# Kernel tuning notes

Hardware: AMD Instinct MI355X
Metric: run time of the kernel (lower is better)

Reference implementation:

```python
import jax, jax.numpy as jnp
import numpy as np

C_S, C_HID, H, P, V = 128, 16, 12, 4, 8
EPS = 1e-08
SOFTPLUS_INV_1 = 0.541324854612918


def _pts_from_linear(x, n_pts):
    # torch: split [..., 3*n] into 3 chunks of n, stack on dim=-1 -> [..., n, 3]
    B, N = x.shape[:2]
    return jnp.moveaxis(x.reshape(B, N, 3, n_pts), -2, -1)


def setup_inputs() -> dict:
    key = jax.random.key(0)
    ks = jax.random.split(key, 16)
    B, N = 2, 512
    hc = H * C_HID            # 192
    hpq = H * P * 3           # 144
    hpkv = H * (P + V) * 3    # 432
    cat_dim = H * (C_HID + V * 4)  # 576
    sc = 0.02
    inp = {
        "s": jax.random.normal(ks[0], (B, N, C_S), jnp.float32),
        "R": jax.random.normal(ks[1], (B, N, 3, 3), jnp.float32),
        "t": jax.random.normal(ks[2], (B, N, 3), jnp.float32),
        "pair_mask": jnp.ones((B, N, N), jnp.float32),
        "Wq": jax.random.normal(ks[3], (C_S, hc), jnp.float32) * sc,
        "bq": jnp.zeros((hc,), jnp.float32),
        "Wkv": jax.random.normal(ks[4], (C_S, 2 * hc), jnp.float32) * sc,
        "bkv": jnp.zeros((2 * hc,), jnp.float32),
        "Wqp": jax.random.normal(ks[5], (C_S, hpq), jnp.float32) * sc,
        "bqp": jnp.zeros((hpq,), jnp.float32),
        "Wkvp": jax.random.normal(ks[6], (C_S, hpkv), jnp.float32) * sc,
        "bkvp": jnp.zeros((hpkv,), jnp.float32),
        "head_weights": jnp.full((H,), SOFTPLUS_INV_1, jnp.float32),
        "Wout": jax.random.normal(ks[7], (cat_dim, C_S), jnp.float32) * sc,
        "bout": jnp.zeros((C_S,), jnp.float32),
    }
    return inp


def reference(s, R, t, pair_mask, Wq, bq, Wkv, bkv, Wqp, bqp, Wkvp, bkvp,
              head_weights, Wout, bout):
    B, N, _ = s.shape
    # scalar q/k/v
    q = (s @ Wq + bq).reshape(B, N, H, C_HID)
    kv = (s @ Wkv + bkv).reshape(B, N, H, 2 * C_HID)
    k, v = kv[..., :C_HID], kv[..., C_HID:]

    # point q/k/v in global frame: R x + t
    qp = _pts_from_linear(s @ Wqp + bqp, H * P)           # [B,N,HP,3]
    qp = jnp.einsum('bnij,bnpj->bnpi', R, qp) + t[:, :, None]
    qp = qp.reshape(B, N, H, P, 3)
    kvp = _pts_from_linear(s @ Wkvp + bkvp, H * (P + V))  # [B,N,H(P+V),3]
    kvp = jnp.einsum('bnij,bnpj->bnpi', R, kvp) + t[:, :, None]
    kvp = kvp.reshape(B, N, H, P + V, 3)
    kp, vp = kvp[..., :P, :], kvp[..., P:, :]

    # scalar attention logits [B,H,N,N]
    a = jnp.einsum('bihc,bjhc->bhij', q, k) * (1.0 / np.sqrt(3 * C_HID))

    # point-distance bias: sum_p ||q_i - k_j||^2 via |q|^2+|k|^2-2q.k
    sq_q = jnp.sum(qp * qp, axis=(-1, -2))   # [B,N,H]
    sq_k = jnp.sum(kp * kp, axis=(-1, -2))   # [B,N,H]
    cross = jnp.einsum('bihpc,bjhpc->bhij', qp, kp)
    d2 = (jnp.swapaxes(sq_q, 1, 2)[..., :, None]
          + jnp.swapaxes(sq_k, 1, 2)[..., None, :]
          - 2.0 * cross)                      # [B,H,N,N]
    hw = jax.nn.softplus(head_weights) * np.sqrt(1.0 / (3 * (P * 9.0 / 2)))
    pt_att = d2 * hw[None, :, None, None] * (-0.5)

    square_mask = 100000.0 * (pair_mask - 1.0)            # [B,N,N]
    a = jax.nn.softmax(a + pt_att + square_mask[:, None], axis=-1)

    # scalar output
    o = jnp.einsum('bhij,bjhc->bihc', a, v).reshape(B, N, H * C_HID)

    # point output, rotated back to local frame: R^T (x - t) form -> R^T x - t
    o_pt = jnp.einsum('bhij,bjhvc->bihvc', a, vp)         # [B,N,H,V,3]
    o_pt = jnp.einsum('bnji,bnhvj->bnhvi', R, o_pt) - t[:, :, None, None]
    o_pt_norm = jnp.sqrt(jnp.sum(o_pt * o_pt, axis=-1) + EPS).reshape(B, N, H * V)
    o_pt_flat = o_pt.reshape(B, N, H * V, 3)

    cat = jnp.concatenate(
        [o, o_pt_flat[..., 0], o_pt_flat[..., 1], o_pt_flat[..., 2], o_pt_norm],
        axis=-1)                                           # [B,N,576]
    return cat @ Wout + bout
```

## Files before the change

### kernel.cpp

```cpp
#include <hip/hip_runtime.h>
#include <hip/hip_bf16.h>
#include <math.h>

#define H_    12
#define B_    2
#define N_    512
#define BH_   (B_*H_)
#define QSCALE 0.14433756729740643f
#define CPT_K  0.13608276348795434f

#define OFF_WPP  1245184
#define OFF_WOP  1318912
#define OFF_BIA  1355776
#define OFF_QB   1356928
#define OFF_KP   1553536
#define OFF_VP   1750144
#define OFF_SA   2045056
#define OFF_SB   2057344
#define OFF_CATP 2069632

typedef __attribute__((ext_vector_type(8))) short sh8;
typedef __attribute__((ext_vector_type(4))) float f32x4;
typedef unsigned short u16t;

static __device__ __forceinline__ u16t f2b(float x) {
    __hip_bfloat16 h = __float2bfloat16(x);
    return *reinterpret_cast<u16t*>(&h);
}
static __device__ __forceinline__ int catp_idx(int tok, int col) {
    return (tok >> 4)*9216 + (col >> 5)*512 + ((col >> 3) & 3)*128
         + (tok & 15)*8 + (col & 7);
}

__global__ __launch_bounds__(256) void convert_kernel(
    const float* __restrict__ Wq,  const float* __restrict__ bq,
    const float* __restrict__ Wkv, const float* __restrict__ bkv,
    const float* __restrict__ Wqp, const float* __restrict__ bqp,
    const float* __restrict__ Wkvp,const float* __restrict__ bkvp,
    const float* __restrict__ Wout, float* __restrict__ ws)
{
    const int g = blockIdx.x * 256 + threadIdx.x;
    union { sh8 v; u16t u[8]; } pk;

    if (g < 18432) {
        int u = g;
        int n = u & 63, kq = (u >> 6) & 3, ks = (u >> 8) & 3, nt = u >> 10;
        int col = nt*64 + n, k0 = ks*32 + kq*8;
        const float* w; int lc, od;
        if (col < 192)      { w = Wq;   lc = col;     od = 192; }
        else if (col < 576) { w = Wkv;  lc = col-192; od = 384; }
        else if (col < 720) { w = Wqp;  lc = col-576; od = 144; }
        else                { w = Wkvp; lc = col-720; od = 432; }
        #pragma unroll
        for (int j = 0; j < 8; ++j) pk.u[j] = f2b(w[(k0+j)*od + lc]);
        *((sh8*)((u16t*)(ws + OFF_WPP)) + u) = pk.v;
    } else if (g < 27648) {
        int u = g - 18432;
        int n = u & 63, kq = (u >> 6) & 3, rem = u >> 8;
        int ks = rem % 18, nt = rem / 18;
        int col = nt*64 + n, k0 = ks*32 + kq*8;
        #pragma unroll
        for (int j = 0; j < 8; ++j) pk.u[j] = f2b(Wout[(k0+j)*128 + col]);
        *((sh8*)((u16t*)(ws + OFF_WOP)) + u) = pk.v;
    } else if (g < 28800) {
        int col = g - 27648;
        float bv;
        if (col < 192)      bv = bq[col];
        else if (col < 576) bv = bkv[col-192];
        else if (col < 720) bv = bqp[col-576];
        else                bv = bkvp[col-720];
        ws[OFF_BIA + col] = bv;
    }
}

__global__ __launch_bounds__(512) void projpack_kernel(
    const float* __restrict__ s,
    const float* __restrict__ Rg, const float* __restrict__ tg,
    const float* __restrict__ hwg, float* __restrict__ ws)
{
    __shared__ float ldsP[8][1160];

    u16t* Qb = (u16t*)(ws + OFF_QB);
    u16t* Kp = (u16t*)(ws + OFF_KP);
    u16t* Vp = (u16t*)(ws + OFF_VP);
    float* sa_g = ws + OFF_SA;
    float* sb_g = ws + OFF_SB;

    const int tid  = threadIdx.x;
    const int w    = tid >> 6, lane = tid & 63;
    const int kq   = lane >> 4, lx = lane & 15;
    const int tok0 = blockIdx.x * 8;
    const int b    = tok0 >> 9, n0 = tok0 & 511;

    sh8 afr[4];
    #pragma unroll
    for (int ks = 0; ks < 4; ++ks) {
        const float* src = s + (tok0 + (lx & 7))*128 + ks*32 + kq*8;
        float4 u0 = *(const float4*)(src);
        float4 u1 = *(const float4*)(src+4);
        union { sh8 v; u16t u[8]; } pk;
        pk.u[0]=f2b(u0.x); pk.u[1]=f2b(u0.y); pk.u[2]=f2b(u0.z); pk.u[3]=f2b(u0.w);
        pk.u[4]=f2b(u1.x); pk.u[5]=f2b(u1.y); pk.u[6]=f2b(u1.z); pk.u[7]=f2b(u1.w);
        afr[ks] = pk.v;
    }

    const sh8* Bp = (const sh8*)((const u16t*)(ws + OFF_WPP));
    const float* bias = ws + OFF_BIA;

    #pragma unroll 3
    for (int g = 0; g < 9; ++g) {
        int gg = w*9 + g;
        int nt = gg >> 2, nq = gg & 3;
        f32x4 acc = {0.f,0.f,0.f,0.f};
        #pragma unroll
        for (int ks = 0; ks < 4; ++ks) {
            sh8 bf = Bp[((nt*4 + ks)*4 + kq)*64 + nq*16 + lx];
            acc = __builtin_amdgcn_mfma_f32_16x16x32_bf16(afr[ks], bf, acc, 0, 0, 0);
        }
        float bv = bias[gg*16 + lx];
        if (kq < 2) {
            #pragma unroll
            for (int r = 0; r < 4; ++r)
                ldsP[kq*4 + r][gg*16 + lx] = acc[r] + bv;
        }
    }
    __syncthreads();

    for (int idx = tid; idx < 8*48; idx += 512) {
        int tk = idx / 48, p = idx % 48;
        int tok = tok0 + tk;
        const float* Rr = Rg + tok*9;
        const float* tr = tg + tok*3;
        float x0 = ldsP[tk][576 +  0 + p];
        float x1 = ldsP[tk][576 + 48 + p];
        float x2 = ldsP[tk][576 + 96 + p];
        ldsP[tk][576 +  0 + p] = Rr[0]*x0 + Rr[1]*x1 + Rr[2]*x2 + tr[0];
        ldsP[tk][576 + 48 + p] = Rr[3]*x0 + Rr[4]*x1 + Rr[5]*x2 + tr[1];
        ldsP[tk][576 + 96 + p] = Rr[6]*x0 + Rr[7]*x1 + Rr[8]*x2 + tr[2];
    }
    for (int idx = tid; idx < 8*144; idx += 512) {
        int tk = idx / 144, p = idx % 144;
        int tok = tok0 + tk;
        const float* Rr = Rg + tok*9;
        const float* tr = tg + tok*3;
        float x0 = ldsP[tk][720 +   0 + p];
        float x1 = ldsP[tk][720 + 144 + p];
        float x2 = ldsP[tk][720 + 288 + p];
        ldsP[tk][720 +   0 + p] = Rr[0]*x0 + Rr[1]*x1 + Rr[2]*x2 + tr[0];
        ldsP[tk][720 + 144 + p] = Rr[3]*x0 + Rr[4]*x1 + Rr[5]*x2 + tr[1];
        ldsP[tk][720 + 288 + p] = Rr[6]*x0 + Rr[7]*x1 + Rr[8]*x2 + tr[2];
    }
    __syncthreads();

    for (int idx = tid; idx < 8*24; idx += 512) {
        int tk = idx / 24, r2 = idx % 24, h = r2 >> 1, half = r2 & 1;
        float hx = hwg[h];
        float sp = (hx > 20.f) ? hx : log1pf(__expf(hx));
        float c_pt = -0.5f * sp * CPT_K;
        union { sh8 v[2]; u16t u[16]; } pk;
        if (half == 0) {
            #pragma unroll
            for (int e = 0; e < 16; ++e) pk.u[e] = f2b(ldsP[tk][h*16 + e] * QSCALE);
        } else {
            float qs = -2.f * c_pt;
            #pragma unroll
            for (int e = 0; e < 12; ++e)
                pk.u[e] = f2b(ldsP[tk][576 + (e%3)*48 + h*4 + e/3] * qs);
            pk.u[12]=0; pk.u[13]=0; pk.u[14]=0; pk.u[15]=0;
        }
        u16t* dst = Qb + ((b*H_+h)*N_ + n0 + tk)*32 + half*16;
        *(sh8*)dst = pk.v[0];
        *(sh8*)(dst+8) = pk.v[1];
    }
    for (int idx = tid; idx < 8*48; idx += 512) {
        int tk = idx / 48, r2 = idx % 48, h = r2 >> 2, fq = r2 & 3;
        int j = n0 + tk, bh = b*H_ + h;
        union { sh8 v; u16t u[8]; } pk;
        #pragma unroll
        for (int e = 0; e < 8; ++e) {
            int c = fq*8 + e;
            float val;
            if (c < 16)      val = ldsP[tk][192 + h*32 + c];
            else if (c < 28) val = ldsP[tk][720 + ((c-16)%3)*144 + h*12 + (c-16)/3];
            else             val = 0.f;
            pk.u[e] = f2b(val);
        }
        *(sh8*)(Kp + bh*16384 + (j>>4)*512 + fq*128 + (j&15)*8) = pk.v;
    }
    for (int idx = tid; idx < 480; idx += 512) {
        int h = idx / 40, d = idx % 40;
        int bh = b*H_ + h;
        union { sh8 v; u16t u[8]; } pk;
        #pragma unroll
        for (int e = 0; e < 8; ++e) {
            float val;
            if (d < 16) val = ldsP[e][192 + h*32 + 16 + d];
            else        val = ldsP[e][720 + ((d-16)%3)*144 + h*12 + 4 + (d-16)/3];
            pk.u[e] = f2b(val);
        }
        int j = n0;
        *(sh8*)(Vp + bh*24576 + (j>>5)*1536 + (d>>4)*512 + ((j>>3)&3)*128
                + (d&15)*8) = pk.v;
    }
    for (int idx = tid; idx < 8*12; idx += 512) {
        int tk = idx / 12, h = idx % 12;
        float hx = hwg[h];
        float sp = (hx > 20.f) ? hx : log1pf(__expf(hx));
        float c_pt = -0.5f * sp * CPT_K;
        float sq = 0.f, sk = 0.f;
        #pragma unroll
        for (int pp = 0; pp < 4; ++pp)
            #pragma unroll
            for (int c = 0; c < 3; ++c) {
                float a = ldsP[tk][576 + c*48  + h*4  + pp]; sq += a*a;
                float k = ldsP[tk][720 + c*144 + h*12 + pp]; sk += k*k;
            }
        sa_g[(b*H_+h)*N_ + n0 + tk] = c_pt * sq;
        sb_g[(b*H_+h)*N_ + n0 + tk] = c_pt * sk;
    }
}

__global__ __launch_bounds__(512, 2) void attn_kernel(
    const float* __restrict__ Rg, const float* __restrict__ tg,
    const float* __restrict__ maskg, float* __restrict__ ws)
{
    __shared__ u16t smP[8*16*72];
    __shared__ float mbuf[3*128*20];
    __shared__ float obuf[32*32];

    const u16t* Qb = (const u16t*)(ws + OFF_QB);
    const u16t* Kp = (const u16t*)(ws + OFF_KP);
    const u16t* Vp = (const u16t*)(ws + OFF_VP);
    const float* sa_g = ws + OFF_SA;
    const float* sb_g = ws + OFF_SB;
    u16t* catp = (u16t*)(ws + OFF_CATP);

    const int tid  = threadIdx.x;
    const int w    = tid >> 6, lane = tid & 63;
    const int rg   = w & 1, jh = w >> 1;
    const int kq   = lane >> 4, lx = lane & 15;
    const int bh   = blockIdx.x >> 4;
    const int it   = blockIdx.x & 15;
    const int b    = bh / H_, h = bh % H_;
    const int i0   = it * 32;

    sh8 qfrag = *(const sh8*)(Qb + (bh*N_ + i0 + rg*16 + lx)*32 + kq*8);
    float sa_r[4];
    #pragma unroll
    for (int r = 0; r < 4; ++r)
        sa_r[r] = sa_g[bh*N_ + i0 + rg*16 + kq*4 + r];

    float m_run[4] = {-1e30f,-1e30f,-1e30f,-1e30f};
    float l_run[4] = {0.f,0.f,0.f,0.f};
    f32x4 oc0 = {0.f,0.f,0.f,0.f}, oc1 = oc0, oc2 = oc0;

    const float* mrow = maskg + (size_t)(b*N_ + i0 + rg*16 + kq*4)*N_ + lx;
    u16t* pw = smP + w*1152;

    #pragma unroll
    for (int t = 0; t < 2; ++t) {
        const int jt = jh*2 + t;
        const int j0 = jt * 64;

        f32x4 sc[4];
        #pragma unroll
        for (int st = 0; st < 4; ++st) {
            sh8 kf = *(const sh8*)(Kp + bh*16384 + (jt*4+st)*512 + kq*128 + lx*8);
            f32x4 z = {0.f,0.f,0.f,0.f};
            sc[st] = __builtin_amdgcn_mfma_f32_16x16x32_bf16(qfrag, kf, z, 0, 0, 0);
        }
        float sbv[4];
        #pragma unroll
        for (int st = 0; st < 4; ++st) sbv[st] = sb_g[bh*N_ + j0 + st*16 + lx];
        float mb[16];
        #pragma unroll
        for (int r = 0; r < 4; ++r)
            #pragma unroll
            for (int st = 0; st < 4; ++st)
                mb[r*4+st] = mrow[r*N_ + j0 + st*16];

        float L[16];
        #pragma unroll
        for (int st = 0; st < 4; ++st)
            #pragma unroll
            for (int r = 0; r < 4; ++r)
                L[st*4+r] = sc[st][r] + sa_r[r] + sbv[st] + 1e5f*(mb[r*4+st] - 1.f);

        #pragma unroll
        for (int r = 0; r < 4; ++r) {
            float tm = fmaxf(fmaxf(L[0*4+r], L[1*4+r]), fmaxf(L[2*4+r], L[3*4+r]));
            tm = fmaxf(tm, __shfl_xor(tm, 1));
            tm = fmaxf(tm, __shfl_xor(tm, 2));
            tm = fmaxf(tm, __shfl_xor(tm, 4));
            tm = fmaxf(tm, __shfl_xor(tm, 8));
            float mnew = fmaxf(m_run[r], tm);
            float al = __expf(m_run[r] - mnew);
            m_run[r] = mnew;
            l_run[r] *= al;
            oc0[r] *= al; oc1[r] *= al; oc2[r] *= al;
        }
        #pragma unroll
        for (int st = 0; st < 4; ++st)
            #pragma unroll
            for (int r = 0; r < 4; ++r) {
                float p = __expf(L[st*4+r] - m_run[r]);
                l_run[r] += p;
                pw[(kq*4+r)*72 + st*16 + lx] = f2b(p);
            }
        #pragma unroll
        for (int c = 0; c < 2; ++c) {
            sh8 pa = *(const sh8*)(pw + lx*72 + c*32 + kq*8);
            #pragma unroll
            for (int nq = 0; nq < 3; ++nq) {
                sh8 vf = *(const sh8*)(Vp + bh*24576 + (jt*2+c)*1536 + nq*512
                                        + kq*128 + lx*8);
                if (nq == 0) oc0 = __builtin_amdgcn_mfma_f32_16x16x32_bf16(pa, vf, oc0, 0,0,0);
                if (nq == 1) oc1 = __builtin_amdgcn_mfma_f32_16x16x32_bf16(pa, vf, oc1, 0,0,0);
                if (nq == 2) oc2 = __builtin_amdgcn_mfma_f32_16x16x32_bf16(pa, vf, oc2, 0,0,0);
            }
        }
    }

    if (jh > 0) {
        float* mb = mbuf + ((jh-1)*128 + rg*64 + lane)*20;
        #pragma unroll
        for (int r = 0; r < 4; ++r) {
            mb[r]      = m_run[r];
            mb[4 + r]  = l_run[r];
            mb[8 + r]  = oc0[r];
            mb[12 + r] = oc1[r];
            mb[16 + r] = oc2[r];
        }
    }
    __syncthreads();
    if (jh == 0) {
        float linv[4];
        #pragma unroll
        for (int r = 0; r < 4; ++r) {
            float ms = m_run[r];
            #pragma unroll
            for (int q = 0; q < 3; ++q)
                ms = fmaxf(ms, mbuf[(q*128 + rg*64 + lane)*20 + r]);
            float eA = __expf(m_run[r] - ms);
            float l = l_run[r]*eA;
            oc0[r] *= eA; oc1[r] *= eA; oc2[r] *= eA;
            #pragma unroll
            for (int q = 0; q < 3; ++q) {
                const float* mb = mbuf + (q*128 + rg*64 + lane)*20;
                float e = __expf(mb[r] - ms);
                l      += mb[4+r]*e;
                oc0[r] += mb[8+r]*e;
                oc1[r] += mb[12+r]*e;
                oc2[r] += mb[16+r]*e;
            }
            l += __shfl_xor(l, 1); l += __shfl_xor(l, 2);
            l += __shfl_xor(l, 4); l += __shfl_xor(l, 8);
            linv[r] = 1.f / l;
        }

        #pragma unroll
        for (int r = 0; r < 4; ++r) {
            int tok = b*N_ + i0 + rg*16 + kq*4 + r;
            catp[catp_idx(tok, h*16 + lx)] = f2b(oc0[r] * linv[r]);
            obuf[(rg*16 + kq*4 + r)*32 + lx]      = oc1[r] * linv[r];
            obuf[(rg*16 + kq*4 + r)*32 + 16 + lx] = oc2[r] * linv[r];
        }

        #pragma unroll
        for (int tsk = 0; tsk < 2; ++tsk) {
            int task = lane + tsk*64;
            int r = task >> 3, pv = task & 7;
            int tok = b*N_ + i0 + rg*16 + r;
            const float* Rr = Rg + tok*9;
            const float* tr = tg + tok*3;
            float g0 = obuf[(rg*16 + r)*32 + pv*3 + 0];
            float g1 = obuf[(rg*16 + r)*32 + pv*3 + 1];
            float g2 = obuf[(rg*16 + r)*32 + pv*3 + 2];
            float px = Rr[0]*g0 + Rr[3]*g1 + Rr[6]*g2 - tr[0];
            float py = Rr[1]*g0 + Rr[4]*g1 + Rr[7]*g2 - tr[1];
            float pz = Rr[2]*g0 + Rr[5]*g1 + Rr[8]*g2 - tr[2];
            float nrm = sqrtf(px*px + py*py + pz*pz + 1e-8f);
            catp[catp_idx(tok, 192 + h*8 + pv)] = f2b(px);
            catp[catp_idx(tok, 288 + h*8 + pv)] = f2b(py);
            catp[catp_idx(tok, 384 + h*8 + pv)] = f2b(pz);
            catp[catp_idx(tok, 480 + h*8 + pv)] = f2b(nrm);
        }
    }
}

__global__ __launch_bounds__(512) void out_kernel(
    const float* __restrict__ bout, const float* __restrict__ ws,
    float* __restrict__ out)
{
    __shared__ float part[2][3][64][4];

    const int tid = threadIdx.x;
    const int w = tid >> 6, lane = tid & 63;
    const int cg = w & 1, kh = w >> 1;
    const int lx = lane & 15, kq = lane >> 4;
    const int nt = blockIdx.x, mt = blockIdx.y;

    const sh8* Ap = (const sh8*)((const u16t*)(ws + OFF_CATP));
    const sh8* Bp = (const sh8*)((const u16t*)(ws + OFF_WOP));

    const int ke0 = (kh*18) >> 2;
    const int ke1 = ((kh+1)*18) >> 2;

    f32x4 acc = {0.f,0.f,0.f,0.f};
    #pragma unroll 5
    for (int ks = ke0; ks < ke1; ++ks) {
        sh8 af = Ap[((mt*18 + ks)*4 + kq)*16 + lx];
        sh8 bf = Bp[(((nt>>1)*18 + ks)*4 + kq)*64 + (nt&1)*32 + cg*16 + lx];
        acc = __builtin_amdgcn_mfma_f32_16x16x32_bf16(af, bf, acc, 0, 0, 0);
    }
    if (kh > 0) {
        #pragma unroll
        for (int r = 0; r < 4; ++r) part[cg][kh-1][lane][r] = acc[r];
    }
    __syncthreads();
    if (kh == 0) {
        int col = nt*32 + cg*16 + lx;
        float bv = bout[col];
        #pragma unroll
        for (int r = 0; r < 4; ++r) {
            int row = mt*16 + kq*4 + r;
            out[row*128 + col] = acc[r] + part[cg][0][lane][r]
                               + part[cg][1][lane][r] + part[cg][2][lane][r] + bv;
        }
    }
}

extern "C" void kernel_launch(void* const* d_in, const int* in_sizes, int n_in,
                              void* d_out, int out_size, void* d_ws, size_t ws_size,
                              hipStream_t stream) {
    const float* s    = (const float*)d_in[0];
    const float* R    = (const float*)d_in[1];
    const float* t    = (const float*)d_in[2];
    const float* mask = (const float*)d_in[3];
    const float* Wq   = (const float*)d_in[4];
    const float* bq   = (const float*)d_in[5];
    const float* Wkv  = (const float*)d_in[6];
    const float* bkv  = (const float*)d_in[7];
    const float* Wqp  = (const float*)d_in[8];
    const float* bqp  = (const float*)d_in[9];
    const float* Wkvp = (const float*)d_in[10];
    const float* bkvp = (const float*)d_in[11];
    const float* hw   = (const float*)d_in[12];
    const float* Wout = (const float*)d_in[13];
    const float* bout = (const float*)d_in[14];
    float* ws  = (float*)d_ws;
    float* out = (float*)d_out;

    convert_kernel<<<113, 256, 0, stream>>>(Wq, bq, Wkv, bkv,
                                            Wqp, bqp, Wkvp, bkvp, Wout, ws);
    projpack_kernel<<<128, 512, 0, stream>>>(s, R, t, hw, ws);
    attn_kernel<<<BH_*16, 512, 0, stream>>>(R, t, mask, ws);
    out_kernel<<<dim3(4, 64), 512, 0, stream>>>(bout, ws, out);
}
```

Measured before the change: 109.8 us.

## Fuse four kernels into one persistent kernel with atomic grid barriers

Replaces the four separate launches (weight convert, projection/pack, attention, output GEMM) with a single persistent kernel of 384 blocks that separates the phases with a software grid barrier built on an atomic counter. The Wout conversion moves off the critical path and now runs alongside the projection phase. The aim is to remove the launch overhead and inter-kernel gaps of a small workload. The risk is deadlock if not all 384 blocks are co-resident, plus spin-wait cost and lower occupancy from the shared 53 KB LDS buffer and launch bounds.

```diff
diff --git a/kernel.cpp b/kernel.cpp
--- a/kernel.cpp
+++ b/kernel.cpp
@@ -6,6 +6,7 @@
 #define B_    2
 #define N_    512
 #define BH_   (B_*H_)
+#define NB_   384
 #define QSCALE 0.14433756729740643f
 #define CPT_K  0.13608276348795434f
 
@@ -23,6 +24,8 @@
 typedef __attribute__((ext_vector_type(4))) float f32x4;
 typedef unsigned short u16t;
 
+__device__ unsigned int g_bar = 0;
+
 static __device__ __forceinline__ u16t f2b(float x) {
     __hip_bfloat16 h = __float2bfloat16(x);
     return *reinterpret_cast<u16t*>(&h);
@@ -32,400 +35,415 @@
          + (tok & 15)*8 + (col & 7);
 }
 
-__global__ __launch_bounds__(256) void convert_kernel(
+static __device__ __forceinline__ void grid_barrier() {
+    __syncthreads();
+    if (threadIdx.x == 0) {
+        __threadfence();
+        unsigned t = atomicAdd(&g_bar, 1u);
+        unsigned target = t - (t % (unsigned)NB_) + (unsigned)NB_;
+        while (__hip_atomic_load(&g_bar, __ATOMIC_RELAXED,
+                                 __HIP_MEMORY_SCOPE_AGENT) < target)
+            __builtin_amdgcn_s_sleep(2);
+        __threadfence();
+    }
+    __syncthreads();
+}
+
+__global__ __launch_bounds__(512, 4) void fused_kernel(
+    const float* __restrict__ s,
+    const float* __restrict__ Rg, const float* __restrict__ tg,
+    const float* __restrict__ maskg,
     const float* __restrict__ Wq,  const float* __restrict__ bq,
     const float* __restrict__ Wkv, const float* __restrict__ bkv,
     const float* __restrict__ Wqp, const float* __restrict__ bqp,
     const float* __restrict__ Wkvp,const float* __restrict__ bkvp,
-    const float* __restrict__ Wout, float* __restrict__ ws)
+    const float* __restrict__ hwg,
+    const float* __restrict__ Wout, const float* __restrict__ bout,
+    float* __restrict__ ws, float* __restrict__ out)
 {
-    const int g = blockIdx.x * 256 + threadIdx.x;
-    union { sh8 v; u16t u[8]; } pk;
-
-    if (g < 18432) {
-        int u = g;
-        int n = u & 63, kq = (u >> 6) & 3, ks = (u >> 8) & 3, nt = u >> 10;
-        int col = nt*64 + n, k0 = ks*32 + kq*8;
-        const float* w; int lc, od;
-        if (col < 192)      { w = Wq;   lc = col;     od = 192; }
-        else if (col < 576) { w = Wkv;  lc = col-192; od = 384; }
-        else if (col < 720) { w = Wqp;  lc = col-576; od = 144; }
-        else                { w = Wkvp; lc = col-720; od = 432; }
-        #pragma unroll
-        for (int j = 0; j < 8; ++j) pk.u[j] = f2b(w[(k0+j)*od + lc]);
-        *((sh8*)((u16t*)(ws + OFF_WPP)) + u) = pk.v;
-    } else if (g < 27648) {
-        int u = g - 18432;
-        int n = u & 63, kq = (u >> 6) & 3, rem = u >> 8;
-        int ks = rem % 18, nt = rem / 18;
-        int col = nt*64 + n, k0 = ks*32 + kq*8;
-        #pragma unroll
-        for (int j = 0; j < 8; ++j) pk.u[j] = f2b(Wout[(k0+j)*128 + col]);
-        *((sh8*)((u16t*)(ws + OFF_WOP)) + u) = pk.v;
-    } else if (g < 28800) {
-        int col = g - 27648;
-        float bv;
-        if (col < 192)      bv = bq[col];
-        else if (col < 576) bv = bkv[col-192];
-        else if (col < 720) bv = bqp[col-576];
-        else                bv = bkvp[col-720];
-        ws[OFF_BIA + col] = bv;
-    }
-}
-
-__global__ __launch_bounds__(512) void projpack_kernel(
-    const float* __restrict__ s,
-    const float* __restrict__ Rg, const float* __restrict__ tg,
-    const float* __restrict__ hwg, float* __restrict__ ws)
-{
-    __shared__ float ldsP[8][1160];
-
-    u16t* Qb = (u16t*)(ws + OFF_QB);
-    u16t* Kp = (u16t*)(ws + OFF_KP);
-    u16t* Vp = (u16t*)(ws + OFF_VP);
-    float* sa_g = ws + OFF_SA;
-    float* sb_g = ws + OFF_SB;
+    __shared__ __align__(16) char ldsraw[53248];
 
     const int tid  = threadIdx.x;
+    const int bid  = blockIdx.x;
     const int w    = tid >> 6, lane = tid & 63;
     const int kq   = lane >> 4, lx = lane & 15;
-    const int tok0 = blockIdx.x * 8;
-    const int b    = tok0 >> 9, n0 = tok0 & 511;
-
-    sh8 afr[4];
-    #pragma unroll
-    for (int ks = 0; ks < 4; ++ks) {
-        const float* src = s + (tok0 + (lx & 7))*128 + ks*32 + kq*8;
-        float4 u0 = *(const float4*)(src);
-        float4 u1 = *(const float4*)(src+4);
-        union { sh8 v; u16t u[8]; } pk;
-        pk.u[0]=f2b(u0.x); pk.u[1]=f2b(u0.y); pk.u[2]=f2b(u0.z); pk.u[3]=f2b(u0.w);
-        pk.u[4]=f2b(u1.x); pk.u[5]=f2b(u1.y); pk.u[6]=f2b(u1.z); pk.u[7]=f2b(u1.w);
-        afr[ks] = pk.v;
+
+    if (w == 0 && bid < 306) {
+        int task = bid*64 + lane;
+        if (task < 18432) {
+            int u = task;
+            int n = u & 63, kq0 = (u >> 6) & 3, ks = (u >> 8) & 3, nt = u >> 10;
+            int col = nt*64 + n, k0 = ks*32 + kq0*8;
+            const float* wp; int lc, od;
+            if (col < 192)      { wp = Wq;   lc = col;     od = 192; }
+            else if (col < 576) { wp = Wkv;  lc = col-192; od = 384; }
+            else if (col < 720) { wp = Wqp;  lc = col-576; od = 144; }
+            else                { wp = Wkvp; lc = col-720; od = 432; }
+            union { sh8 v; u16t uu[8]; } pk;
+            #pragma unroll
+            for (int j = 0; j < 8; ++j) pk.uu[j] = f2b(wp[(k0+j)*od + lc]);
+            *((sh8*)((u16t*)(ws + OFF_WPP)) + u) = pk.v;
+        } else {
+            int col = task - 18432;
+            float bv;
+            if (col < 192)      bv = bq[col];
+            else if (col < 576) bv = bkv[col-192];
+            else if (col < 720) bv = bqp[col-576];
+            else                bv = bkvp[col-720];
+            ws[OFF_BIA + col] = bv;
+        }
     }
-
-    const sh8* Bp = (const sh8*)((const u16t*)(ws + OFF_WPP));
-    const float* bias = ws + OFF_BIA;
-
-    #pragma unroll 3
-    for (int g = 0; g < 9; ++g) {
-        int gg = w*9 + g;
-        int nt = gg >> 2, nq = gg & 3;
-        f32x4 acc = {0.f,0.f,0.f,0.f};
+    grid_barrier();
+
+    if (bid < 128) {
+        float (*ldsP)[1160] = reinterpret_cast<float(*)[1160]>(ldsraw);
+
+        u16t* Qb = (u16t*)(ws + OFF_QB);
+        u16t* Kp = (u16t*)(ws + OFF_KP);
+        u16t* Vp = (u16t*)(ws + OFF_VP);
+        float* sa_g = ws + OFF_SA;
+        float* sb_g = ws + OFF_SB;
+
+        const int tok0 = bid * 8;
+        const int b    = tok0 >> 9, n0 = tok0 & 511;
+
+        sh8 afr[4];
         #pragma unroll
         for (int ks = 0; ks < 4; ++ks) {
-            sh8 bf = Bp[((nt*4 + ks)*4 + kq)*64 + nq*16 + lx];
-            acc = __builtin_amdgcn_mfma_f32_16x16x32_bf16(afr[ks], bf, acc, 0, 0, 0);
-        }
-        float bv = bias[gg*16 + lx];
-        if (kq < 2) {
-            #pragma unroll
-            for (int r = 0; r < 4; ++r)
-                ldsP[kq*4 + r][gg*16 + lx] = acc[r] + bv;
-        }
+            const float* src = s + (tok0 + (lx & 7))*128 + ks*32 + kq*8;
+            float4 u0 = *(const float4*)(src);
+            float4 u1 = *(const float4*)(src+4);
+            union { sh8 v; u16t u[8]; } pk;
+            pk.u[0]=f2b(u0.x); pk.u[1]=f2b(u0.y); pk.u[2]=f2b(u0.z); pk.u[3]=f2b(u0.w);
+            pk.u[4]=f2b(u1.x); pk.u[5]=f2b(u1.y); pk.u[6]=f2b(u1.z); pk.u[7]=f2b(u1.w);
+            afr[ks] = pk.v;
+        }
+
+        const sh8* Bp = (const sh8*)((const u16t*)(ws + OFF_WPP));
+        const float* bias = ws + OFF_BIA;
+
+        #pragma unroll 3
+        for (int g = 0; g < 9; ++g) {
+            int gg = w*9 + g;
+            int nt = gg >> 2, nq = gg & 3;
+            f32x4 acc = {0.f,0.f,0.f,0.f};
+            #pragma unroll
+            for (int ks = 0; ks < 4; ++ks) {
+                sh8 bf = Bp[((nt*4 + ks)*4 + kq)*64 + nq*16 + lx];
+                acc = __builtin_amdgcn_mfma_f32_16x16x32_bf16(afr[ks], bf, acc, 0, 0, 0);
+            }
+            float bv = bias[gg*16 + lx];
+            if (kq < 2) {
+                #pragma unroll
+                for (int r = 0; r < 4; ++r)
+                    ldsP[kq*4 + r][gg*16 + lx] = acc[r] + bv;
+            }
+        }
+        __syncthreads();
+
+        for (int idx = tid; idx < 8*48; idx += 512) {
+            int tk = idx / 48, p = idx % 48;
+            int tok = tok0 + tk;
+            const float* Rr = Rg + tok*9;
+            const float* tr = tg + tok*3;
+            float x0 = ldsP[tk][576 +  0 + p];
+            float x1 = ldsP[tk][576 + 48 + p];
+            float x2 = ldsP[tk][576 + 96 + p];
+            ldsP[tk][576 +  0 + p] = Rr[0]*x0 + Rr[1]*x1 + Rr[2]*x2 + tr[0];
+            ldsP[tk][576 + 48 + p] = Rr[3]*x0 + Rr[4]*x1 + Rr[5]*x2 + tr[1];
+            ldsP[tk][576 + 96 + p] = Rr[6]*x0 + Rr[7]*x1 + Rr[8]*x2 + tr[2];
+        }
+        for (int idx = tid; idx < 8*144; idx += 512) {
+            int tk = idx / 144, p = idx % 144;
+            int tok = tok0 + tk;
+            const float* Rr = Rg + tok*9;
+            const float* tr = tg + tok*3;
+            float x0 = ldsP[tk][720 +   0 + p];
+            float x1 = ldsP[tk][720 + 144 + p];
+            float x2 = ldsP[tk][720 + 288 + p];
+            ldsP[tk][720 +   0 + p] = Rr[0]*x0 + Rr[1]*x1 + Rr[2]*x2 + tr[0];
+            ldsP[tk][720 + 144 + p] = Rr[3]*x0 + Rr[4]*x1 + Rr[5]*x2 + tr[1];
+            ldsP[tk][720 + 288 + p] = Rr[6]*x0 + Rr[7]*x1 + Rr[8]*x2 + tr[2];
+        }
+        __syncthreads();
+
+        for (int idx = tid; idx < 8*24; idx += 512) {
+            int tk = idx / 24, r2 = idx % 24, h = r2 >> 1, half = r2 & 1;
+            float hx = hwg[h];
+            float sp = (hx > 20.f) ? hx : log1pf(__expf(hx));
+            float c_pt = -0.5f * sp * CPT_K;
+            union { sh8 v[2]; u16t u[16]; } pk;
+            if (half == 0) {
+                #pragma unroll
+                for (int e = 0; e < 16; ++e) pk.u[e] = f2b(ldsP[tk][h*16 + e] * QSCALE);
+            } else {
+                float qs = -2.f * c_pt;
+                #pragma unroll
+                for (int e = 0; e < 12; ++e)
+                    pk.u[e] = f2b(ldsP[tk][576 + (e%3)*48 + h*4 + e/3] * qs);
+                pk.u[12]=0; pk.u[13]=0; pk.u[14]=0; pk.u[15]=0;
+            }
+            u16t* dst = Qb + ((b*H_+h)*N_ + n0 + tk)*32 + half*16;
+            *(sh8*)dst = pk.v[0];
+            *(sh8*)(dst+8) = pk.v[1];
+        }
+        for (int idx = tid; idx < 8*48; idx += 512) {
+            int tk = idx / 48, r2 = idx % 48, h = r2 >> 2, fq = r2 & 3;
+            int j = n0 + tk, bh = b*H_ + h;
+            union { sh8 v; u16t u[8]; } pk;
+            #pragma unroll
+            for (int e = 0; e < 8; ++e) {
+                int c = fq*8 + e;
+                float val;
+                if (c < 16)      val = ldsP[tk][192 + h*32 + c];
+                else if (c < 28) val = ldsP[tk][720 + ((c-16)%3)*144 + h*12 + (c-16)/3];
+                else             val = 0.f;
+                pk.u[e] = f2b(val);
+            }
+            *(sh8*)(Kp + bh*16384 + (j>>4)*512 + fq*128 + (j&15)*8) = pk.v;
+        }
+        for (int idx = tid; idx < 480; idx += 512) {
+            int h = idx / 40, d = idx % 40;
+            int bh = b*H_ + h;
+            union { sh8 v; u16t u[8]; } pk;
+            #pragma unroll
+            for (int e = 0; e < 8; ++e) {
+                float val;
+                if (d < 16) val = ldsP[e][192 + h*32 + 16 + d];
+                else        val = ldsP[e][720 + ((d-16)%3)*144 + h*12 + 4 + (d-16)/3];
+                pk.u[e] = f2b(val);
+            }
+            int j = n0;
+            *(sh8*)(Vp + bh*24576 + (j>>5)*1536 + (d>>4)*512 + ((j>>3)&3)*128
+                    + (d&15)*8) = pk.v;
+        }
+        for (int idx = tid; idx < 8*12; idx += 512) {
+            int tk = idx / 12, h = idx % 12;
+            float hx = hwg[h];
+            float sp = (hx > 20.f) ? hx : log1pf(__expf(hx));
+            float c_pt = -0.5f * sp * CPT_K;
+            float sq = 0.f, sk = 0.f;
+            #pragma unroll
+            for (int pp = 0; pp < 4; ++pp)
+                #pragma unroll
+                for (int c = 0; c < 3; ++c) {
+                    float a = ldsP[tk][576 + c*48  + h*4  + pp]; sq += a*a;
+                    float k = ldsP[tk][720 + c*144 + h*12 + pp]; sk += k*k;
+                }
+            sa_g[(b*H_+h)*N_ + n0 + tk] = c_pt * sq;
+            sb_g[(b*H_+h)*N_ + n0 + tk] = c_pt * sk;
+        }
+    } else if (bid < 272 && w == 0) {
+        int u = (bid - 128)*64 + lane;
+        int n = u & 63, kq0 = (u >> 6) & 3, rem = u >> 8;
+        int ks = rem % 18, nt = rem / 18;
+        int col = nt*64 + n, k0 = ks*32 + kq0*8;
+        union { sh8 v; u16t uu[8]; } pk;
+        #pragma unroll
+        for (int j = 0; j < 8; ++j) pk.uu[j] = f2b(Wout[(k0+j)*128 + col]);
+        *((sh8*)((u16t*)(ws + OFF_WOP)) + u) = pk.v;
     }
-    __syncthreads();
-
-    for (int idx = tid; idx < 8*48; idx += 512) {
-        int tk = idx / 48, p = idx % 48;
-        int tok = tok0 + tk;
-        const float* Rr = Rg + tok*9;
-        const float* tr = tg + tok*3;
-        float x0 = ldsP[tk][576 +  0 + p];
-        float x1 = ldsP[tk][576 + 48 + p];
-        float x2 = ldsP[tk][576 + 96 + p];
-        ldsP[tk][576 +  0 + p] = Rr[0]*x0 + Rr[1]*x1 + Rr[2]*x2 + tr[0];
-        ldsP[tk][576 + 48 + p] = Rr[3]*x0 + Rr[4]*x1 + Rr[5]*x2 + tr[1];
-        ldsP[tk][576 + 96 + p] = Rr[6]*x0 + Rr[7]*x1 + Rr[8]*x2 + tr[2];
-    }
-    for (int idx = tid; idx < 8*144; idx += 512) {
-        int tk = idx / 144, p = idx % 144;
-        int tok = tok0 + tk;
-        const float* Rr = Rg + tok*9;
-        const float* tr = tg + tok*3;
-        float x0 = ldsP[tk][720 +   0 + p];
-        float x1 = ldsP[tk][720 + 144 + p];
-        float x2 = ldsP[tk][720 + 288 + p];
-        ldsP[tk][720 +   0 + p] = Rr[0]*x0 + Rr[1]*x1 + Rr[2]*x2 + tr[0];
-        ldsP[tk][720 + 144 + p] = Rr[3]*x0 + Rr[4]*x1 + Rr[5]*x2 + tr[1];
-        ldsP[tk][720 + 288 + p] = Rr[6]*x0 + Rr[7]*x1 + Rr[8]*x2 + tr[2];
-    }
-    __syncthreads();
-
-    for (int idx = tid; idx < 8*24; idx += 512) {
-        int tk = idx / 24, r2 = idx % 24, h = r2 >> 1, half = r2 & 1;
-        float hx = hwg[h];
-        float sp = (hx > 20.f) ? hx : log1pf(__expf(hx));
-        float c_pt = -0.5f * sp * CPT_K;
-        union { sh8 v[2]; u16t u[16]; } pk;
-        if (half == 0) {
-            #pragma unroll
-            for (int e = 0; e < 16; ++e) pk.u[e] = f2b(ldsP[tk][h*16 + e] * QSCALE);
-        } else {
-            float qs = -2.f * c_pt;
-            #pragma unroll
-            for (int e = 0; e < 12; ++e)
-                pk.u[e] = f2b(ldsP[tk][576 + (e%3)*48 + h*4 + e/3] * qs);
-            pk.u[12]=0; pk.u[13]=0; pk.u[14]=0; pk.u[15]=0;
-        }
-        u16t* dst = Qb + ((b*H_+h)*N_ + n0 + tk)*32 + half*16;
-        *(sh8*)dst = pk.v[0];
-        *(sh8*)(dst+8) = pk.v[1];
-    }
-    for (int idx = tid; idx < 8*48; idx += 512) {
-        int tk = idx / 48, r2 = idx % 48, h = r2 >> 2, fq = r2 & 3;
-        int j = n0 + tk, bh = b*H_ + h;
-        union { sh8 v; u16t u[8]; } pk;
-        #pragma unroll
-        for (int e = 0; e < 8; ++e) {
-            int c = fq*8 + e;
-            float val;
-            if (c < 16)      val = ldsP[tk][192 + h*32 + c];
-            else if (c < 28) val = ldsP[tk][720 + ((c-16)%3)*144 + h*12 + (c-16)/3];
-            else             val = 0.f;
-            pk.u[e] = f2b(val);
-        }
-        *(sh8*)(Kp + bh*16384 + (j>>4)*512 + fq*128 + (j&15)*8) = pk.v;
-    }
-    for (int idx = tid; idx < 480; idx += 512) {
-        int h = idx / 40, d = idx % 40;
-        int bh = b*H_ + h;
-        union { sh8 v; u16t u[8]; } pk;
-        #pragma unroll
-        for (int e = 0; e < 8; ++e) {
-            float val;
-            if (d < 16) val = ldsP[e][192 + h*32 + 16 + d];
-            else        val = ldsP[e][720 + ((d-16)%3)*144 + h*12 + 4 + (d-16)/3];
-            pk.u[e] = f2b(val);
-        }
-        int j = n0;
-        *(sh8*)(Vp + bh*24576 + (j>>5)*1536 + (d>>4)*512 + ((j>>3)&3)*128
-                + (d&15)*8) = pk.v;
-    }
-    for (int idx = tid; idx < 8*12; idx += 512) {
-        int tk = idx / 12, h = idx % 12;
-        float hx = hwg[h];
-        float sp = (hx > 20.f) ? hx : log1pf(__expf(hx));
-        float c_pt = -0.5f * sp * CPT_K;
-        float sq = 0.f, sk = 0.f;
-        #pragma unroll
-        for (int pp = 0; pp < 4; ++pp)
-            #pragma unroll
-            for (int c = 0; c < 3; ++c) {
-                float a = ldsP[tk][576 + c*48  + h*4  + pp]; sq += a*a;
-                float k = ldsP[tk][720 + c*144 + h*12 + pp]; sk += k*k;
-            }
-        sa_g[(b*H_+h)*N_ + n0 + tk] = c_pt * sq;
-        sb_g[(b*H_+h)*N_ + n0 + tk] = c_pt * sk;
-    }
-}
-
-__global__ __launch_bounds__(512, 2) void attn_kernel(
-    const float* __restrict__ Rg, const float* __restrict__ tg,
-    const float* __restrict__ maskg, float* __restrict__ ws)
-{
-    __shared__ u16t smP[8*16*72];
-    __shared__ float mbuf[3*128*20];
-    __shared__ float obuf[32*32];
-
-    const u16t* Qb = (const u16t*)(ws + OFF_QB);
-    const u16t* Kp = (const u16t*)(ws + OFF_KP);
-    const u16t* Vp = (const u16t*)(ws + OFF_VP);
-    const float* sa_g = ws + OFF_SA;
-    const float* sb_g = ws + OFF_SB;
-    u16t* catp = (u16t*)(ws + OFF_CATP);
-
-    const int tid  = threadIdx.x;
-    const int w    = tid >> 6, lane = tid & 63;
-    const int rg   = w & 1, jh = w >> 1;
-    const int kq   = lane >> 4, lx = lane & 15;
-    const int bh   = blockIdx.x >> 4;
-    const int it   = blockIdx.x & 15;
-    const int b    = bh / H_, h = bh % H_;
-    const int i0   = it * 32;
-
-    sh8 qfrag = *(const sh8*)(Qb + (bh*N_ + i0 + rg*16 + lx)*32 + kq*8);
-    float sa_r[4];
-    #pragma unroll
-    for (int r = 0; r < 4; ++r)
-        sa_r[r] = sa_g[bh*N_ + i0 + rg*16 + kq*4 + r];
-
-    float m_run[4] = {-1e30f,-1e30f,-1e30f,-1e30f};
-    float l_run[4] = {0.f,0.f,0.f,0.f};
-    f32x4 oc0 = {0.f,0.f,0.f,0.f}, oc1 = oc0, oc2 = oc0;
-
-    const float* mrow = maskg + (size_t)(b*N_ + i0 + rg*16 + kq*4)*N_ + lx;
-    u16t* pw = smP + w*1152;
-
-    #pragma unroll
-    for (int t = 0; t < 2; ++t) {
-        const int jt = jh*2 + t;
-        const int j0 = jt * 64;
-
-        f32x4 sc[4];
-        #pragma unroll
-        for (int st = 0; st < 4; ++st) {
-            sh8 kf = *(const sh8*)(Kp + bh*16384 + (jt*4+st)*512 + kq*128 + lx*8);
-            f32x4 z = {0.f,0.f,0.f,0.f};
-            sc[st] = __builtin_amdgcn_mfma_f32_16x16x32_bf16(qfrag, kf, z, 0, 0, 0);
-        }
-        float sbv[4];
-        #pragma unroll
-        for (int st = 0; st < 4; ++st) sbv[st] = sb_g[bh*N_ + j0 + st*16 + lx];
-        float mb[16];
+    grid_barrier();
+
+    {
+        u16t* smP  = (u16t*)ldsraw;
+        float* mbuf = (float*)(ldsraw + 18432);
+        float* obuf = (float*)(ldsraw + 49152);
+
+        const u16t* Qb = (const u16t*)(ws + OFF_QB);
+        const u16t* Kp = (const u16t*)(ws + OFF_KP);
+        const u16t* Vp = (const u16t*)(ws + OFF_VP);
+        const float* sa_g = ws + OFF_SA;
+        const float* sb_g = ws + OFF_SB;
+        u16t* catp = (u16t*)(ws + OFF_CATP);
+
+        const int rg   = w & 1, jh = w >> 1;
+        const int bh   = bid >> 4;
+        const int it   = bid & 15;
+        const int b    = bh / H_, h = bh % H_;
+        const int i0   = it * 32;
+
+        sh8 qfrag = *(const sh8*)(Qb + (bh*N_ + i0 + rg*16 + lx)*32 + kq*8);
+        float sa_r[4];
         #pragma unroll
         for (int r = 0; r < 4; ++r)
+            sa_r[r] = sa_g[bh*N_ + i0 + rg*16 + kq*4 + r];
+
+        float m_run[4] = {-1e30f,-1e30f,-1e30f,-1e30f};
+        float l_run[4] = {0.f,0.f,0.f,0.f};
+        f32x4 oc0 = {0.f,0.f,0.f,0.f}, oc1 = oc0, oc2 = oc0;
+
+        const float* mrow = maskg + (size_t)(b*N_ + i0 + rg*16 + kq*4)*N_ + lx;
+        u16t* pw = smP + w*1152;
+
+        #pragma unroll
+        for (int t = 0; t < 2; ++t) {
+            const int jt = jh*2 + t;
+            const int j0 = jt * 64;
+
+            f32x4 sc[4];
+            #pragma unroll
+            for (int st = 0; st < 4; ++st) {
+                sh8 kf = *(const sh8*)(Kp + bh*16384 + (jt*4+st)*512 + kq*128 + lx*8);
+                f32x4 z = {0.f,0.f,0.f,0.f};
+                sc[st] = __builtin_amdgcn_mfma_f32_16x16x32_bf16(qfrag, kf, z, 0, 0, 0);
+            }
+            float sbv[4];
+            #pragma unroll
+            for (int st = 0; st < 4; ++st) sbv[st] = sb_g[bh*N_ + j0 + st*16 + lx];
+            float mb[16];
+            #pragma unroll
+            for (int r = 0; r < 4; ++r)
+                #pragma unroll
+                for (int st = 0; st < 4; ++st)
+                    mb[r*4+st] = mrow[r*N_ + j0 + st*16];
+
+            float L[16];
             #pragma unroll
             for (int st = 0; st < 4; ++st)
-                mb[r*4+st] = mrow[r*N_ + j0 + st*16];
-
-        float L[16];
-        #pragma unroll
-        for (int st = 0; st < 4; ++st)
+                #pragma unroll
+                for (int r = 0; r < 4; ++r)
+                    L[st*4+r] = sc[st][r] + sa_r[r] + sbv[st] + 1e5f*(mb[r*4+st] - 1.f);
+
+            #pragma unroll
+            for (int r = 0; r < 4; ++r) {
+                float tm = fmaxf(fmaxf(L[0*4+r], L[1*4+r]), fmaxf(L[2*4+r], L[3*4+r]));
+                tm = fmaxf(tm, __shfl_xor(tm, 1));
+                tm = fmaxf(tm, __shfl_xor(tm, 2));
+                tm = fmaxf(tm, __shfl_xor(tm, 4));
+                tm = fmaxf(tm, __shfl_xor(tm, 8));
+                float mnew = fmaxf(m_run[r], tm);
+                float al = __expf(m_run[r] - mnew);
+                m_run[r] = mnew;
+                l_run[r] *= al;
+                oc0[r] *= al; oc1[r] *= al; oc2[r] *= al;
+            }
+            #pragma unroll
+            for (int st = 0; st < 4; ++st)
+                #pragma unroll
+                for (int r = 0; r < 4; ++r) {
+                    float p = __expf(L[st*4+r] - m_run[r]);
+                    l_run[r] += p;
+                    pw[(kq*4+r)*72 + st*16 + lx] = f2b(p);
+                }
+            #pragma unroll
+            for (int c = 0; c < 2; ++c) {
+                sh8 pa = *(const sh8*)(pw + lx*72 + c*32 + kq*8);
+                #pragma unroll
+                for (int nq = 0; nq < 3; ++nq) {
+                    sh8 vf = *(const sh8*)(Vp + bh*24576 + (jt*2+c)*1536 + nq*512
+                                            + kq*128 + lx*8);
+                    if (nq == 0) oc0 = __builtin_amdgcn_mfma_f32_16x16x32_bf16(pa, vf, oc0, 0,0,0);
+                    if (nq == 1) oc1 = __builtin_amdgcn_mfma_f32_16x16x32_bf16(pa, vf, oc1, 0,0,0);
+                    if (nq == 2) oc2 = __builtin_amdgcn_mfma_f32_16x16x32_bf16(pa, vf, oc2, 0,0,0);
+                }
+            }
+        }
+
+        if (jh > 0) {
+            float* mb = mbuf + ((jh-1)*128 + rg*64 + lane)*20;
+            #pragma unroll
+            for (int r = 0; r < 4; ++r) {
+                mb[r]      = m_run[r];
+                mb[4 + r]  = l_run[r];
+                mb[8 + r]  = oc0[r];
+                mb[12 + r] = oc1[r];
+                mb[16 + r] = oc2[r];
+            }
+        }
+        __syncthreads();
+        if (jh == 0) {
+            float linv[4];
+            #pragma unroll
+            for (int r = 0; r < 4; ++r) {
+                float ms = m_run[r];
+                #pragma unroll
+                for (int q = 0; q < 3; ++q)
+                    ms = fmaxf(ms, mbuf[(q*128 + rg*64 + lane)*20 + r]);
+                float eA = __expf(m_run[r] - ms);
+                float l = l_run[r]*eA;
+                oc0[r] *= eA; oc1[r] *= eA; oc2[r] *= eA;
+                #pragma unroll
+                for (int q = 0; q < 3; ++q) {
+                    const float* mb = mbuf + (q*128 + rg*64 + lane)*20;
+                    float e = __expf(mb[r] - ms);
+                    l      += mb[4+r]*e;
+                    oc0[r] += mb[8+r]*e;
+                    oc1[r] += mb[12+r]*e;
+                    oc2[r] += mb[16+r]*e;
+                }
+                l += __shfl_xor(l, 1); l += __shfl_xor(l, 2);
+                l += __shfl_xor(l, 4); l += __shfl_xor(l, 8);
+                linv[r] = 1.f / l;
+            }
+
+            #pragma unroll
+            for (int r = 0; r < 4; ++r) {
+                int tok = b*N_ + i0 + rg*16 + kq*4 + r;
+                catp[catp_idx(tok, h*16 + lx)] = f2b(oc0[r] * linv[r]);
+                obuf[(rg*16 + kq*4 + r)*32 + lx]      = oc1[r] * linv[r];
+                obuf[(rg*16 + kq*4 + r)*32 + 16 + lx] = oc2[r] * linv[r];
+            }
+
+            #pragma unroll
+            for (int tsk = 0; tsk < 2; ++tsk) {
+                int task = lane + tsk*64;
+                int r = task >> 3, pv = task & 7;
+                int tok = b*N_ + i0 + rg*16 + r;
+                const float* Rr = Rg + tok*9;
+                const float* tr = tg + tok*3;
+                float g0 = obuf[(rg*16 + r)*32 + pv*3 + 0];
+                float g1 = obuf[(rg*16 + r)*32 + pv*3 + 1];
+                float g2 = obuf[(rg*16 + r)*32 + pv*3 + 2];
+                float px = Rr[0]*g0 + Rr[3]*g1 + Rr[6]*g2 - tr[0];
+                float py = Rr[1]*g0 + Rr[4]*g1 + Rr[7]*g2 - tr[1];
+                float pz = Rr[2]*g0 + Rr[5]*g1 + Rr[8]*g2 - tr[2];
+                float nrm = sqrtf(px*px + py*py + pz*pz + 1e-8f);
+                catp[catp_idx(tok, 192 + h*8 + pv)] = f2b(px);
+                catp[catp_idx(tok, 288 + h*8 + pv)] = f2b(py);
+                catp[catp_idx(tok, 384 + h*8 + pv)] = f2b(pz);
+                catp[catp_idx(tok, 480 + h*8 + pv)] = f2b(nrm);
+            }
+        }
+    }
+    grid_barrier();
+
+    if (bid < 256) {
+        float* part = (float*)ldsraw;
+
+        const int cg = w & 1, kh = w >> 1;
+        const int nt = bid & 3, mt = bid >> 2;
+
+        const sh8* Ap = (const sh8*)((const u16t*)(ws + OFF_CATP));
+        const sh8* Bp = (const sh8*)((const u16t*)(ws + OFF_WOP));
+
+        const int ke0 = (kh*18) >> 2;
+        const int ke1 = ((kh+1)*18) >> 2;
+
+        f32x4 acc = {0.f,0.f,0.f,0.f};
+        #pragma unroll 5
+        for (int ks = ke0; ks < ke1; ++ks) {
+            sh8 af = Ap[((mt*18 + ks)*4 + kq)*16 + lx];
+            sh8 bf = Bp[(((nt>>1)*18 + ks)*4 + kq)*64 + (nt&1)*32 + cg*16 + lx];
+            acc = __builtin_amdgcn_mfma_f32_16x16x32_bf16(af, bf, acc, 0, 0, 0);
+        }
+        if (kh > 0) {
             #pragma unroll
             for (int r = 0; r < 4; ++r)
-                L[st*4+r] = sc[st][r] + sa_r[r] + sbv[st] + 1e5f*(mb[r*4+st] - 1.f);
-
-        #pragma unroll
-        for (int r = 0; r < 4; ++r) {
-            float tm = fmaxf(fmaxf(L[0*4+r], L[1*4+r]), fmaxf(L[2*4+r], L[3*4+r]));
-            tm = fmaxf(tm, __shfl_xor(tm, 1));
-            tm = fmaxf(tm, __shfl_xor(tm, 2));
-            tm = fmaxf(tm, __shfl_xor(tm, 4));
-            tm = fmaxf(tm, __shfl_xor(tm, 8));
-            float mnew = fmaxf(m_run[r], tm);
-            float al = __expf(m_run[r] - mnew);
-            m_run[r] = mnew;
-            l_run[r] *= al;
-            oc0[r] *= al; oc1[r] *= al; oc2[r] *= al;
-        }
-        #pragma unroll
-        for (int st = 0; st < 4; ++st)
+                part[((cg*3 + (kh-1))*64 + lane)*4 + r] = acc[r];
+        }
+        __syncthreads();
+        if (kh == 0) {
+            int col = nt*32 + cg*16 + lx;
+            float bv = bout[col];
             #pragma unroll
             for (int r = 0; r < 4; ++r) {
-                float p = __expf(L[st*4+r] - m_run[r]);
-                l_run[r] += p;
-                pw[(kq*4+r)*72 + st*16 + lx] = f2b(p);
-            }
-        #pragma unroll
-        for (int c = 0; c < 2; ++c) {
-            sh8 pa = *(const sh8*)(pw + lx*72 + c*32 + kq*8);
-            #pragma unroll
-            for (int nq = 0; nq < 3; ++nq) {
-                sh8 vf = *(const sh8*)(Vp + bh*24576 + (jt*2+c)*1536 + nq*512
-                                        + kq*128 + lx*8);
-                if (nq == 0) oc0 = __builtin_amdgcn_mfma_f32_16x16x32_bf16(pa, vf, oc0, 0,0,0);
-                if (nq == 1) oc1 = __builtin_amdgcn_mfma_f32_16x16x32_bf16(pa, vf, oc1, 0,0,0);
-                if (nq == 2) oc2 = __builtin_amdgcn_mfma_f32_16x16x32_bf16(pa, vf, oc2, 0,0,0);
-            }
-        }
-    }
-
-    if (jh > 0) {
-        float* mb = mbuf + ((jh-1)*128 + rg*64 + lane)*20;
-        #pragma unroll
-        for (int r = 0; r < 4; ++r) {
-            mb[r]      = m_run[r];
-            mb[4 + r]  = l_run[r];
-            mb[8 + r]  = oc0[r];
-            mb[12 + r] = oc1[r];
-            mb[16 + r] = oc2[r];
-        }
-    }
-    __syncthreads();
-    if (jh == 0) {
-        float linv[4];
-        #pragma unroll
-        for (int r = 0; r < 4; ++r) {
-            float ms = m_run[r];
-            #pragma unroll
-            for (int q = 0; q < 3; ++q)
-                ms = fmaxf(ms, mbuf[(q*128 + rg*64 + lane)*20 + r]);
-            float eA = __expf(m_run[r] - ms);
-            float l = l_run[r]*eA;
-            oc0[r] *= eA; oc1[r] *= eA; oc2[r] *= eA;
-            #pragma unroll
-            for (int q = 0; q < 3; ++q) {
-                const float* mb = mbuf + (q*128 + rg*64 + lane)*20;
-                float e = __expf(mb[r] - ms);
-                l      += mb[4+r]*e;
-                oc0[r] += mb[8+r]*e;
-                oc1[r] += mb[12+r]*e;
-                oc2[r] += mb[16+r]*e;
-            }
-            l += __shfl_xor(l, 1); l += __shfl_xor(l, 2);
-            l += __shfl_xor(l, 4); l += __shfl_xor(l, 8);
-            linv[r] = 1.f / l;
-        }
-
-        #pragma unroll
-        for (int r = 0; r < 4; ++r) {
-            int tok = b*N_ + i0 + rg*16 + kq*4 + r;
-            catp[catp_idx(tok, h*16 + lx)] = f2b(oc0[r] * linv[r]);
-            obuf[(rg*16 + kq*4 + r)*32 + lx]      = oc1[r] * linv[r];
-            obuf[(rg*16 + kq*4 + r)*32 + 16 + lx] = oc2[r] * linv[r];
-        }
-
-        #pragma unroll
-        for (int tsk = 0; tsk < 2; ++tsk) {
-            int task = lane + tsk*64;
-            int r = task >> 3, pv = task & 7;
-            int tok = b*N_ + i0 + rg*16 + r;
-            const float* Rr = Rg + tok*9;
-            const float* tr = tg + tok*3;
-            float g0 = obuf[(rg*16 + r)*32 + pv*3 + 0];
-            float g1 = obuf[(rg*16 + r)*32 + pv*3 + 1];
-            float g2 = obuf[(rg*16 + r)*32 + pv*3 + 2];
-            float px = Rr[0]*g0 + Rr[3]*g1 + Rr[6]*g2 - tr[0];
-            float py = Rr[1]*g0 + Rr[4]*g1 + Rr[7]*g2 - tr[1];
-            float pz = Rr[2]*g0 + Rr[5]*g1 + Rr[8]*g2 - tr[2];
-            float nrm = sqrtf(px*px + py*py + pz*pz + 1e-8f);
-            catp[catp_idx(tok, 192 + h*8 + pv)] = f2b(px);
-            catp[catp_idx(tok, 288 + h*8 + pv)] = f2b(py);
-            catp[catp_idx(tok, 384 + h*8 + pv)] = f2b(pz);
-            catp[catp_idx(tok, 480 + h*8 + pv)] = f2b(nrm);
-        }
-    }
-}
-
-__global__ __launch_bounds__(512) void out_kernel(
-    const float* __restrict__ bout, const float* __restrict__ ws,
-    float* __restrict__ out)
-{
-    __shared__ float part[2][3][64][4];
-
-    const int tid = threadIdx.x;
-    const int w = tid >> 6, lane = tid & 63;
-    const int cg = w & 1, kh = w >> 1;
-    const int lx = lane & 15, kq = lane >> 4;
-    const int nt = blockIdx.x, mt = blockIdx.y;
-
-    const sh8* Ap = (const sh8*)((const u16t*)(ws + OFF_CATP));
-    const sh8* Bp = (const sh8*)((const u16t*)(ws + OFF_WOP));
-
-    const int ke0 = (kh*18) >> 2;
-    const int ke1 = ((kh+1)*18) >> 2;
-
-    f32x4 acc = {0.f,0.f,0.f,0.f};
-    #pragma unroll 5
-    for (int ks = ke0; ks < ke1; ++ks) {
-        sh8 af = Ap[((mt*18 + ks)*4 + kq)*16 + lx];
-        sh8 bf = Bp[(((nt>>1)*18 + ks)*4 + kq)*64 + (nt&1)*32 + cg*16 + lx];
-        acc = __builtin_amdgcn_mfma_f32_16x16x32_bf16(af, bf, acc, 0, 0, 0);
-    }
-    if (kh > 0) {
-        #pragma unroll
-        for (int r = 0; r < 4; ++r) part[cg][kh-1][lane][r] = acc[r];
-    }
-    __syncthreads();
-    if (kh == 0) {
-        int col = nt*32 + cg*16 + lx;
-        float bv = bout[col];
-        #pragma unroll
-        for (int r = 0; r < 4; ++r) {
-            int row = mt*16 + kq*4 + r;
-            out[row*128 + col] = acc[r] + part[cg][0][lane][r]
-                               + part[cg][1][lane][r] + part[cg][2][lane][r] + bv;
+                int row = mt*16 + kq*4 + r;
+                out[row*128 + col] = acc[r]
+                                   + part[((cg*3 + 0)*64 + lane)*4 + r]
+                                   + part[((cg*3 + 1)*64 + lane)*4 + r]
+                                   + part[((cg*3 + 2)*64 + lane)*4 + r] + bv;
+            }
         }
     }
 }
@@ -451,9 +469,7 @@
     float* ws  = (float*)d_ws;
     float* out = (float*)d_out;
 
-    convert_kernel<<<113, 256, 0, stream>>>(Wq, bq, Wkv, bkv,
-                                            Wqp, bqp, Wkvp, bkvp, Wout, ws);
-    projpack_kernel<<<128, 512, 0, stream>>>(s, R, t, hw, ws);
-    attn_kernel<<<BH_*16, 512, 0, stream>>>(R, t, mask, ws);
-    out_kernel<<<dim3(4, 64), 512, 0, stream>>>(bout, ws, out);
+    fused_kernel<<<NB_, 512, 0, stream>>>(s, R, t, mask, Wq, bq, Wkv, bkv,
+                                          Wqp, bqp, Wkvp, bkvp, hw, Wout, bout,
+                                          ws, out);
 }
```

Measured after the change: 214.4 us. +95.3%, slower.
